# Kernel optimization log

Hardware: AMD Instinct MI355X
Metric: run time of the kernel (lower is better)

## Reference

```python
import jax, jax.numpy as jnp
import numpy as np

NUM_HEADS = 12
LATENT = 768
HEAD_DIM = LATENT // NUM_HEADS
SCALE = float(np.sqrt(LATENT))  # note: sqrt(latent_vector_size), not sqrt(head_dim), per source


def setup_inputs() -> dict:
    key = jax.random.key(0)
    ks = jax.random.split(key, 7)
    B, S, D = 8, 1024, LATENT
    std = 1.0 / np.sqrt(D)
    return {
        "x": jax.random.normal(ks[0], (B, S, D), dtype=jnp.float32),
        "Wq": jax.random.normal(ks[1], (D, D), dtype=jnp.float32) * std,
        "bq": jnp.zeros((D,), dtype=jnp.float32),
        "Wk": jax.random.normal(ks[2], (D, D), dtype=jnp.float32) * std,
        "bk": jnp.zeros((D,), dtype=jnp.float32),
        "Wv": jax.random.normal(ks[3], (D, D), dtype=jnp.float32) * std,
        "bv": jnp.zeros((D,), dtype=jnp.float32),
    }


def reference(x, Wq, bq, Wk, bk, Wv, bv):
    B, S, D = x.shape
    H, Hd = NUM_HEADS, HEAD_DIM
    # torch Linear: y = x @ W.T + b
    q = (x @ Wq.T + bq).reshape(B, S, H, Hd).transpose(0, 2, 1, 3)  # [B,H,S,Hd]
    k = (x @ Wk.T + bk).reshape(B, S, H, Hd).transpose(0, 2, 1, 3)
    v = (x @ Wv.T + bv).reshape(B, S, H, Hd).transpose(0, 2, 1, 3)
    qk = jnp.einsum("bhsd,bhtd->bhst", q, k) / SCALE  # [B,H,S,S]
    A = jax.nn.softmax(qk, axis=-1)
    # dropout(0.1) treated as eval-mode identity
    out = jnp.einsum("bhst,bhtd->bhsd", A, v)  # [B,H,S,Hd]
    out = out.transpose(0, 2, 1, 3).reshape(B, S, D)
    return (out, A)
```

## Files before the change

kernel.cpp:

```cpp
#include <hip/hip_runtime.h>
#include <stdint.h>

typedef __bf16 bf16_t;
typedef __bf16 bf16x4 __attribute__((ext_vector_type(4)));
typedef __bf16 bf16x8 __attribute__((ext_vector_type(8)));
typedef float f32x4 __attribute__((ext_vector_type(4)));

#define MFMA(a, b, c) __builtin_amdgcn_mfma_f32_16x16x32_bf16(a, b, c, 0, 0, 0)

__device__ __forceinline__ float fexp2(float x) { return __builtin_amdgcn_exp2f(x); }

typedef __attribute__((address_space(3))) uint32_t as3_u32;
typedef __attribute__((address_space(1))) uint32_t as1_u32;
__device__ __forceinline__ void gload_lds16(const void* g, void* l) {
  __builtin_amdgcn_global_load_lds((as1_u32*)g, (as3_u32*)l, 16, 0, 0);
}

__global__ void cvt_all(const float* __restrict__ x, const float* __restrict__ wq,
                        const float* __restrict__ wk, const float* __restrict__ wv,
                        bf16_t* __restrict__ dst) {
  int i = blockIdx.x * blockDim.x + threadIdx.x;
  if (i >= 2015232) return;
  const float* src; int off;
  if (i < 1572864) { src = x; off = i; }
  else {
    int j = i - 1572864;
    if (j < 147456)      { src = wq; off = j; }
    else if (j < 294912) { src = wk; off = j - 147456; }
    else                 { src = wv; off = j - 294912; }
  }
  const f32x4 v = reinterpret_cast<const f32x4*>(src)[off];
  bf16x4 o = { (bf16_t)v.x, (bf16_t)v.y, (bf16_t)v.z, (bf16_t)v.w };
  reinterpret_cast<bf16x4*>(dst)[i] = o;
}

__global__ __launch_bounds__(256)
void qkv_gemm(const bf16_t* __restrict__ X, const bf16_t* __restrict__ Wb,
              const float* __restrict__ bq, const float* __restrict__ bk,
              const float* __restrict__ bv,
              bf16_t* __restrict__ Qo, bf16_t* __restrict__ Ko, bf16_t* __restrict__ Vo)
{
  __shared__ __align__(16) bf16_t smem[17408];
  bf16_t* const sA0 = smem;
  bf16_t* const sA1 = smem + 4096;
  bf16_t* const sB0 = smem + 8192;
  bf16_t* const sB1 = smem + 12288;
  bf16_t* const ep  = smem;

  const int tid = threadIdx.x;
  const int lane = tid & 63, w = tid >> 6;
  const int wr = w >> 1, wc = w & 1;
  const int lq = lane & 15, lg = lane >> 4;
  const int m0 = blockIdx.x * 128;
  const int n0 = blockIdx.y * 128;
  const int z  = blockIdx.z;

  const bf16_t* W = Wb + z * 589824;
  const float* bias = (z == 0) ? bq : (z == 1) ? bk : bv;

  const int arow = wr * 64, brow = wc * 64;
  const int sr = tid >> 2, scc = (tid & 3) * 8;

  const bf16_t* gA = X + (m0 + sr) * 768 + scc;
  const bf16_t* gB = W + (n0 + sr) * 768 + scc;
  const int ko = lg * 8;

  f32x4 acc[4][4] = {};

#define STAGE(bufA, bufB, kt)                                            \
  do {                                                                   \
    const int kk_ = (kt) * 32;                                           \
    gload_lds16(gA + kk_,             &bufA[tid * 8]);                   \
    gload_lds16(gA + kk_ + 64 * 768,  &bufA[(tid + 256) * 8]);           \
    gload_lds16(gB + kk_,             &bufB[tid * 8]);                   \
    gload_lds16(gB + kk_ + 64 * 768,  &bufB[(tid + 256) * 8]);           \
  } while (0)

#define COMPUTE(bufA, bufB)                                              \
  do {                                                                   \
    bf16x8 af[4], bfr[4];                                                \
    _Pragma("unroll")                                                    \
    for (int mf = 0; mf < 4; ++mf)                                       \
      af[mf] = *(const bf16x8*)&bufA[(arow + mf * 16 + lq) * 32 + ko];   \
    _Pragma("unroll")                                                    \
    for (int nf = 0; nf < 4; ++nf)                                       \
      bfr[nf] = *(const bf16x8*)&bufB[(brow + nf * 16 + lq) * 32 + ko];  \
    _Pragma("unroll")                                                    \
    for (int mf = 0; mf < 4; ++mf)                                       \
      _Pragma("unroll")                                                  \
      for (int nf = 0; nf < 4; ++nf)                                     \
        acc[mf][nf] = MFMA(af[mf], bfr[nf], acc[mf][nf]);                \
  } while (0)

  STAGE(sA0, sB0, 0);
  for (int kt = 0; kt < 24; kt += 2) {
    __syncthreads();
    STAGE(sA1, sB1, kt + 1);
    COMPUTE(sA0, sB0);
    __syncthreads();
    if (kt + 2 < 24) STAGE(sA0, sB0, kt + 2);
    COMPUTE(sA1, sB1);
  }
  __syncthreads();

  const int b = m0 >> 10, sq0 = m0 & 1023;

  if (z < 2) {
#pragma unroll
    for (int nf = 0; nf < 4; ++nf) {
      const int c = brow + nf * 16 + lq;
      const float bval = bias[n0 + c];
#pragma unroll
      for (int mf = 0; mf < 4; ++mf)
#pragma unroll
        for (int jr = 0; jr < 4; ++jr)
          ep[(arow + mf * 16 + lg * 4 + jr) * 136 + c] = (bf16_t)(acc[mf][nf][jr] + bval);
    }
    __syncthreads();
    bf16_t* dst = (z == 0) ? Qo : Ko;
#pragma unroll
    for (int nh = 0; nh < 2; ++nh) {
      const int h = (n0 >> 6) + nh;
#pragma unroll
      for (int rp = 0; rp < 2; ++rp) {
        const int r = (tid >> 2) + rp * 64;
        bf16_t* o = dst + ((size_t)(b * 12 + h) * 1024 + sq0 + r) * 64;
        const bf16_t* s = &ep[r * 136 + nh * 64];
#pragma unroll
        for (int i = 0; i < 2; ++i) {
          const int ch = (tid & 3) + i * 4;
          *(bf16x8*)(o + ch * 8) = *(const bf16x8*)(s + ch * 8);
        }
      }
    }
  } else {
#pragma unroll
    for (int nf = 0; nf < 4; ++nf) {
      const int c = brow + nf * 16 + lq;
      const float bval = bias[n0 + c];
#pragma unroll
      for (int mf = 0; mf < 4; ++mf) {
        const int r0 = arow + mf * 16 + lg * 4;
        bf16x4 pv = { (bf16_t)(acc[mf][nf][0] + bval), (bf16_t)(acc[mf][nf][1] + bval),
                      (bf16_t)(acc[mf][nf][2] + bval), (bf16_t)(acc[mf][nf][3] + bval) };
        *(bf16x4*)&ep[c * 136 + r0] = pv;
      }
    }
    __syncthreads();
    const int c = tid >> 1;
    const int h = (n0 >> 6) + (c >> 6), dd = c & 63;
    bf16_t* o = Vo + ((size_t)(b * 12 + h) * 64 + dd) * 1024 + sq0;
    const bf16_t* s = &ep[c * 136];
#pragma unroll
    for (int i = 0; i < 8; ++i) {
      const int ch = (tid & 1) + i * 2;
      *(bf16x8*)(o + ch * 8) = *(const bf16x8*)(s + ch * 8);
    }
  }
#undef STAGE
#undef COMPUTE
}

__global__ __launch_bounds__(512)
void attn_kernel(const bf16_t* __restrict__ Q, const bf16_t* __restrict__ K,
                 const bf16_t* __restrict__ V, float* __restrict__ out,
                 float* __restrict__ Aout)
{
  __shared__ __align__(16) bf16_t Pl[32 * 1032];
  __shared__ __align__(16) bf16_t Ql[32 * 72];
  __shared__ float red[8][32];
  __shared__ float inv_s[32];

  const int tid = threadIdx.x, lane = tid & 63, w = tid >> 6;
  const int lq = lane & 15, lg = lane >> 4;
  const int bh = blockIdx.x, q0 = blockIdx.y * 32;

  const bf16_t* Qp = Q + (bh * 1024 + q0) * 64;
  const bf16_t* Kp = K + bh * 1024 * 64;
  const bf16_t* Vt = V + bh * 64 * 1024;

  if (tid < 256) {
    const int q = tid >> 3, du = (tid & 7) * 8;
    *(bf16x8*)&Ql[q * 72 + du] = *(const bf16x8*)(Qp + q * 64 + du);
  }
  __syncthreads();

  const float CEXP = 1.4426950408889634f / 27.712812921102035f;

  bf16x8 bqf[2][2];
#pragma unroll
  for (int dh = 0; dh < 2; ++dh)
#pragma unroll
    for (int qf = 0; qf < 2; ++qf)
      bqf[dh][qf] = *(const bf16x8*)&Ql[(qf * 16 + lq) * 72 + dh * 32 + lg * 8];

  float psum0 = 0.f, psum1 = 0.f;

  for (int i = 0; i < 2; ++i) {
    const int t0 = (w + i * 8) * 64;
    bf16x8 af[4][2];
#pragma unroll
    for (int mf = 0; mf < 4; ++mf) {
      const bf16_t* kp = Kp + (t0 + mf * 16 + lq) * 64 + lg * 8;
      af[mf][0] = *(const bf16x8*)(kp);
      af[mf][1] = *(const bf16x8*)(kp + 32);
    }
#pragma unroll
    for (int mf = 0; mf < 4; ++mf) {
#pragma unroll
      for (int qf = 0; qf < 2; ++qf) {
        f32x4 acc = {};
        acc = MFMA(af[mf][0], bqf[0][qf], acc);
        acc = MFMA(af[mf][1], bqf[1][qf], acc);
        float p0 = fexp2(acc[0] * CEXP);
        float p1 = fexp2(acc[1] * CEXP);
        float p2 = fexp2(acc[2] * CEXP);
        float p3 = fexp2(acc[3] * CEXP);
        if (qf == 0) psum0 += p0 + p1 + p2 + p3;
        else         psum1 += p0 + p1 + p2 + p3;
        bf16x4 pv = { (bf16_t)p0, (bf16_t)p1, (bf16_t)p2, (bf16_t)p3 };
        const int q = qf * 16 + lq;
        const int tt = t0 + mf * 16 + lg * 4;
        *(bf16x4*)&Pl[q * 1032 + tt] = pv;
      }
    }
  }

  psum0 += __shfl_xor(psum0, 16); psum0 += __shfl_xor(psum0, 32);
  psum1 += __shfl_xor(psum1, 16); psum1 += __shfl_xor(psum1, 32);
  if (lane < 16) { red[w][lane] = psum0; red[w][16 + lane] = psum1; }
  __syncthreads();
  if (tid < 32) {
    float s = 0.f;
#pragma unroll
    for (int j = 0; j < 8; ++j) s += red[j][tid];
    inv_s[tid] = 1.0f / s;
  }
  __syncthreads();

  const int dq = w & 3, kh = w >> 2;
  const int r4 = 4 * w;
  float* const Ap0 = Aout + ((size_t)bh * 1024 + q0) * 1024;

  f32x4 oacc[2] = {};
  for (int ks = 0; ks < 16; ++ks) {
    const int kc = (kh * 16 + ks) * 32;
    bf16x8 vb = *(const bf16x8*)(Vt + (dq * 16 + lq) * 1024 + kc + lg * 8);
#pragma unroll
    for (int mf = 0; mf < 2; ++mf) {
      bf16x8 pa = *(const bf16x8*)&Pl[(mf * 16 + lq) * 1032 + kc + lg * 8];
      oacc[mf] = MFMA(pa, vb, oacc[mf]);
    }
    const int ar = r4 + (ks & 3);
    const int cc = (ks >> 2) * 256;
    const float ainv = inv_s[ar];
    bf16x4 pv = *(const bf16x4*)&Pl[ar * 1032 + cc + lane * 4];
    f32x4 o = { (float)pv[0] * ainv, (float)pv[1] * ainv,
                (float)pv[2] * ainv, (float)pv[3] * ainv };
    __builtin_nontemporal_store(o, (f32x4*)(Ap0 + (size_t)ar * 1024 + cc + lane * 4));
  }

  __syncthreads();
  float* const Ol = (float*)Pl;
#pragma unroll
  for (int mf = 0; mf < 2; ++mf)
#pragma unroll
    for (int jr = 0; jr < 4; ++jr) {
      const int q = mf * 16 + lg * 4 + jr;
      Ol[kh * 2176 + q * 68 + dq * 16 + lq] = oacc[mf][jr];
    }
  __syncthreads();
  {
    const int b = bh / 12, h = bh % 12;
    const int r = tid >> 4, c4 = (tid & 15) * 4;
    const float s = inv_s[r];
    f32x4 p0 = *(const f32x4*)&Ol[r * 68 + c4];
    f32x4 p1 = *(const f32x4*)&Ol[2176 + r * 68 + c4];
    f32x4 o = { (p0[0] + p1[0]) * s, (p0[1] + p1[1]) * s,
                (p0[2] + p1[2]) * s, (p0[3] + p1[3]) * s };
    *(f32x4*)(out + ((size_t)b * 1024 + q0 + r) * 768 + h * 64 + c4) = o;
  }
}

extern "C" void kernel_launch(void* const* d_in, const int* in_sizes, int n_in,
                              void* d_out, int out_size, void* d_ws, size_t ws_size,
                              hipStream_t stream) {
  (void)in_sizes; (void)n_in; (void)out_size; (void)ws_size;
  const float* x  = (const float*)d_in[0];
  const float* Wq = (const float*)d_in[1];
  const float* bq = (const float*)d_in[2];
  const float* Wk = (const float*)d_in[3];
  const float* bk = (const float*)d_in[4];
  const float* Wv = (const float*)d_in[5];
  const float* bv = (const float*)d_in[6];

  float* out  = (float*)d_out;
  float* Aout = out + 6291456;

  bf16_t* ws   = (bf16_t*)d_ws;
  bf16_t* x_bf = ws;
  bf16_t* w_bf = ws + 6291456;
  bf16_t* q_ws = ws + 8060928;
  bf16_t* k_ws = ws + 14352384;
  bf16_t* v_ws = ws + 20643840;

  cvt_all<<<7872, 256, 0, stream>>>(x, Wq, Wk, Wv, ws);
  qkv_gemm<<<dim3(64, 6, 3), 256, 0, stream>>>(x_bf, w_bf, bq, bk, bv, q_ws, k_ws, v_ws);
  attn_kernel<<<dim3(96, 32), 512, 0, stream>>>(q_ws, k_ws, v_ws, out, Aout);
}
```

Measured before the change: 170.0 us.

## Compute PV per-wave on own key slice before softmax normalization barrier

Each wave now keeps its P tile in a private LDS region and multiplies it by V for its own key columns right after computing exp, before the block-wide sum barrier. Partial outputs from all eight waves are then combined with LDS atomicAdd into a zeroed buffer. The aim is to overlap the PV matmul with the exp phase and remove the dependency on the full shared P matrix. In exchange it adds LDS atomics, an extra zeroing pass and barrier, and more accumulator registers, and the A-output reads now gather across the per-wave layout.

```diff
diff --git a/kernel.cpp b/kernel.cpp
--- a/kernel.cpp
+++ b/kernel.cpp
@@ -166,7 +166,7 @@
                  const bf16_t* __restrict__ V, float* __restrict__ out,
                  float* __restrict__ Aout)
 {
-  __shared__ __align__(16) bf16_t Pl[32 * 1032];
+  __shared__ __align__(16) bf16_t Pw[8 * 32 * 136];
   __shared__ __align__(16) bf16_t Ql[32 * 72];
   __shared__ float red[8][32];
   __shared__ float inv_s[32];
@@ -194,6 +194,7 @@
     for (int qf = 0; qf < 2; ++qf)
       bqf[dh][qf] = *(const bf16x8*)&Ql[(qf * 16 + lq) * 72 + dh * 32 + lg * 8];
 
+  bf16_t* const Pww = Pw + w * 4352;
   float psum0 = 0.f, psum1 = 0.f;
 
   for (int i = 0; i < 2; ++i) {
@@ -219,9 +220,26 @@
         if (qf == 0) psum0 += p0 + p1 + p2 + p3;
         else         psum1 += p0 + p1 + p2 + p3;
         bf16x4 pv = { (bf16_t)p0, (bf16_t)p1, (bf16_t)p2, (bf16_t)p3 };
-        const int q = qf * 16 + lq;
-        const int tt = t0 + mf * 16 + lg * 4;
-        *(bf16x4*)&Pl[q * 1032 + tt] = pv;
+        *(bf16x4*)&Pww[(qf * 16 + lq) * 136 + i * 64 + mf * 16 + lg * 4] = pv;
+      }
+    }
+  }
+
+  f32x4 oacc[2][4] = {};
+  for (int i = 0; i < 2; ++i) {
+    const int t0 = (w + i * 8) * 64;
+#pragma unroll
+    for (int kw = 0; kw < 2; ++kw) {
+      bf16x8 pa[2];
+#pragma unroll
+      for (int mf = 0; mf < 2; ++mf)
+        pa[mf] = *(const bf16x8*)&Pww[(mf * 16 + lq) * 136 + i * 64 + kw * 32 + lg * 8];
+#pragma unroll
+      for (int db = 0; db < 4; ++db) {
+        bf16x8 vb = *(const bf16x8*)(Vt + (db * 16 + lq) * 1024 + t0 + kw * 32 + lg * 8);
+#pragma unroll
+        for (int mf = 0; mf < 2; ++mf)
+          oacc[mf][db] = MFMA(pa[mf], vb, oacc[mf][db]);
       }
     }
   }
@@ -238,46 +256,41 @@
   }
   __syncthreads();
 
-  const int dq = w & 3, kh = w >> 2;
   const int r4 = 4 * w;
   float* const Ap0 = Aout + ((size_t)bh * 1024 + q0) * 1024;
-
-  f32x4 oacc[2] = {};
   for (int ks = 0; ks < 16; ++ks) {
-    const int kc = (kh * 16 + ks) * 32;
-    bf16x8 vb = *(const bf16x8*)(Vt + (dq * 16 + lq) * 1024 + kc + lg * 8);
-#pragma unroll
-    for (int mf = 0; mf < 2; ++mf) {
-      bf16x8 pa = *(const bf16x8*)&Pl[(mf * 16 + lq) * 1032 + kc + lg * 8];
-      oacc[mf] = MFMA(pa, vb, oacc[mf]);
-    }
     const int ar = r4 + (ks & 3);
     const int cc = (ks >> 2) * 256;
     const float ainv = inv_s[ar];
-    bf16x4 pv = *(const bf16x4*)&Pl[ar * 1032 + cc + lane * 4];
+    const int t = cc + lane * 4;
+    const int w2 = (t >> 6) & 7, i2 = t >> 9, loc = t & 63;
+    bf16x4 pv = *(const bf16x4*)&Pw[(w2 * 32 + ar) * 136 + i2 * 64 + loc];
     f32x4 o = { (float)pv[0] * ainv, (float)pv[1] * ainv,
                 (float)pv[2] * ainv, (float)pv[3] * ainv };
-    __builtin_nontemporal_store(o, (f32x4*)(Ap0 + (size_t)ar * 1024 + cc + lane * 4));
-  }
-
-  __syncthreads();
-  float* const Ol = (float*)Pl;
+    __builtin_nontemporal_store(o, (f32x4*)(Ap0 + (size_t)ar * 1024 + t));
+  }
+
+  __syncthreads();
+  float* const Ol = (float*)Pw;
+  for (int idx = tid; idx < 2176; idx += 512) Ol[idx] = 0.f;
+  __syncthreads();
 #pragma unroll
   for (int mf = 0; mf < 2; ++mf)
 #pragma unroll
-    for (int jr = 0; jr < 4; ++jr) {
-      const int q = mf * 16 + lg * 4 + jr;
-      Ol[kh * 2176 + q * 68 + dq * 16 + lq] = oacc[mf][jr];
-    }
+    for (int db = 0; db < 4; ++db)
+#pragma unroll
+      for (int jr = 0; jr < 4; ++jr) {
+        const int q = mf * 16 + lg * 4 + jr;
+        const int d = db * 16 + lq;
+        atomicAdd(&Ol[q * 68 + d], oacc[mf][db][jr]);
+      }
   __syncthreads();
   {
     const int b = bh / 12, h = bh % 12;
     const int r = tid >> 4, c4 = (tid & 15) * 4;
     const float s = inv_s[r];
-    f32x4 p0 = *(const f32x4*)&Ol[r * 68 + c4];
-    f32x4 p1 = *(const f32x4*)&Ol[2176 + r * 68 + c4];
-    f32x4 o = { (p0[0] + p1[0]) * s, (p0[1] + p1[1]) * s,
-                (p0[2] + p1[2]) * s, (p0[3] + p1[3]) * s };
+    f32x4 p = *(const f32x4*)&Ol[r * 68 + c4];
+    f32x4 o = { p[0] * s, p[1] * s, p[2] * s, p[3] * s };
     *(f32x4*)(out + ((size_t)b * 1024 + q0 + r) * 768 + h * 64 + c4) = o;
   }
 }
```

Result: slower. 413.8 us (+143.4%).
